# Kernel optimization log

Measured on AMD Instinct MI355X. Metric: run time of the kernel, lower is better.

Reference implementation:

```python
import jax, jax.numpy as jnp
import numpy as np

N = 50000      # nodes
E = 800000     # edges (avg degree 16)
IN = 128       # in_channels
H = 128        # hidden_channels
K = 20         # n_clusters
ALPHA = 0.2


def _glorot(key, shape):
    lim = float(np.sqrt(6.0 / (shape[0] + shape[1])))
    return jax.random.uniform(key, shape, jnp.float32, -lim, lim)


def setup_inputs() -> dict:
    key = jax.random.key(0)
    ks = jax.random.split(key, 12)
    x = jax.random.normal(ks[0], (N, IN), jnp.float32)
    edge_index = jax.random.randint(ks[1], (2, E), 0, N, dtype=jnp.int64)
    edge_weight = jax.random.uniform(ks[2], (E,), jnp.float32)
    perm = jax.random.permutation(ks[3], N).astype(jnp.int64)
    W1 = _glorot(ks[4], (IN, H)); b1 = jnp.zeros((H,), jnp.float32)
    W2 = _glorot(ks[5], (H, H));  b2 = jnp.zeros((H,), jnp.float32)
    W3 = _glorot(ks[6], (H, H));  b3 = jnp.zeros((H,), jnp.float32)
    W4 = _glorot(ks[7], (H, H));  b4 = jnp.zeros((H,), jnp.float32)
    prelu_a = jnp.full((H,), 0.25, jnp.float32)
    Wc = _glorot(ks[8], (H, IN)); bc = jnp.zeros((IN,), jnp.float32)
    mu = jax.random.normal(ks[9], (K, IN), jnp.float32)
    return dict(x=x, edge_index=edge_index, edge_weight=edge_weight, perm=perm,
                W1=W1, b1=b1, W2=W2, b2=b2, W3=W3, b3=b3, W4=W4, b4=b4,
                prelu_a=prelu_a, Wc=Wc, bc=bc, mu=mu)


def _gcn_norm(src, dst, ew, n):
    # add self-loops (weight 1) + symmetric normalization, PyG gcn_norm
    loop = jnp.arange(n)
    src2 = jnp.concatenate([src, loop])
    dst2 = jnp.concatenate([dst, loop])
    w2 = jnp.concatenate([ew, jnp.ones((n,), ew.dtype)])
    deg = jax.ops.segment_sum(w2, dst2, num_segments=n)
    dinv = jnp.where(deg > 0, jax.lax.rsqrt(deg), 0.0)
    norm = dinv[src2] * w2 * dinv[dst2]
    return src2, dst2, norm


def _gcn_conv(x, W, b, src2, dst2, norm, n):
    h = x @ W                              # [n, out]
    msg = h[src2] * norm[:, None]          # gather + scale
    return jax.ops.segment_sum(msg, dst2, num_segments=n) + b


def reference(x, edge_index, edge_weight, perm, W1, b1, W2, b2, W3, b3, W4, b4,
              prelu_a, Wc, bc, mu):
    n = x.shape[0]
    src, dst = edge_index[0], edge_index[1]
    src2, dst2, norm = _gcn_norm(src, dst, edge_weight, n)

    def encoder(h):
        h = _gcn_conv(h, W1, b1, src2, dst2, norm, n)
        h = _gcn_conv(h, W2, b2, src2, dst2, norm, n)
        h = _gcn_conv(h, W3, b3, src2, dst2, norm, n)
        h = _gcn_conv(h, W4, b4, src2, dst2, norm, n)
        return jnp.where(h >= 0, h, prelu_a * h)  # PReLU

    pos_z = encoder(x)
    neg_z = encoder(x[perm])                       # corruption: permute node rows
    summary = jax.nn.sigmoid(pos_z.mean(axis=0))   # [H]

    x_out = _gcn_conv(pos_z, Wc, bc, src2, dst2, norm, n)  # [N, IN]

    # Student's-t soft assignment: ||x_i - mu_k||^2 via expansion (same math)
    d = (jnp.sum(x_out * x_out, axis=1, keepdims=True)
         + jnp.sum(mu * mu, axis=1)[None, :]
         - 2.0 * (x_out @ mu.T))
    d = jnp.maximum(d, 0.0)
    q = 1.0 / (1.0 + d / ALPHA + 1e-8)
    q = q ** (ALPHA + 1.0) / 2.0
    q = q / jnp.sum(q, axis=1, keepdims=True)
    return pos_z, neg_z, summary, x_out, q
```

## Files before the change

kernel.cpp:

```cpp
#include <hip/hip_runtime.h>
#include <hip/hip_bf16.h>

constexpr int NN = 50000;
constexpr int EE = 800000;
constexpr int C  = 128;
constexpr int KC = 20;
constexpr int NB = (NN + 1023) / 1024;

typedef __attribute__((ext_vector_type(8))) short bf16x8;
typedef __attribute__((ext_vector_type(4))) float f32x4;

__device__ inline unsigned short f2bf(float f) {
    unsigned u = __float_as_uint(f);
    u += 0x7fff + ((u >> 16) & 1);
    return (unsigned short)(u >> 16);
}
__device__ inline float bf2f(unsigned short h) {
    return __uint_as_float(((unsigned)h) << 16);
}


__global__ void k_hist(const int* __restrict__ ei, unsigned* cnt) {
    int e = blockIdx.x * 256 + threadIdx.x;
    if (e >= EE) return;
    atomicAdd(&cnt[ei[EE + e]], 1u);
}

__global__ __launch_bounds__(256) void k_scan1(const unsigned* __restrict__ cnt,
                                               unsigned* __restrict__ bsum) {
    __shared__ unsigned red[256];
    int b = blockIdx.x, t = threadIdx.x;
    int i0 = b * 1024 + t * 4;
    unsigned s = 0;
    #pragma unroll
    for (int j = 0; j < 4; ++j) { int i = i0 + j; s += (i < NN) ? cnt[i] : 0u; }
    red[t] = s; __syncthreads();
    for (int st = 128; st > 0; st >>= 1) { if (t < st) red[t] += red[t + st]; __syncthreads(); }
    if (t == 0) bsum[b] = red[0];
}

__global__ void k_scan2(unsigned* bsum, unsigned* total) {
    int t = threadIdx.x;
    unsigned v = (t < NB) ? bsum[t] : 0u;
    unsigned x = v;
    #pragma unroll
    for (int s = 1; s < 64; s <<= 1) { unsigned u = __shfl_up(x, s, 64); if (t >= s) x += u; }
    if (t < NB) bsum[t] = x - v;
    if (t == 63) *total = x;
}

__global__ __launch_bounds__(256) void k_scan3(const unsigned* __restrict__ cnt,
                                               const unsigned* __restrict__ bsum,
                                               const unsigned* __restrict__ total,
                                               unsigned* __restrict__ off,
                                               unsigned* __restrict__ cursor) {
    __shared__ unsigned wred[4];
    int b = blockIdx.x, t = threadIdx.x, lane = t & 63, wv = t >> 6;
    int i0 = b * 1024 + t * 4;
    unsigned v[4]; unsigned s = 0;
    #pragma unroll
    for (int j = 0; j < 4; ++j) { int i = i0 + j; v[j] = (i < NN) ? cnt[i] : 0u; s += v[j]; }
    unsigned x = s;
    #pragma unroll
    for (int st = 1; st < 64; st <<= 1) { unsigned u = __shfl_up(x, st, 64); if (lane >= st) x += u; }
    if (lane == 63) wred[wv] = x;
    __syncthreads();
    unsigned woff = 0;
    for (int k = 0; k < 4; ++k) if (k < wv) woff += wred[k];
    unsigned excl = bsum[b] + woff + x - s;
    #pragma unroll
    for (int j = 0; j < 4; ++j) {
        int i = i0 + j;
        if (i < NN) { off[i] = excl; cursor[i] = excl; excl += v[j]; }
    }
    if (b == 0 && t == 0) off[NN] = *total;
}

__global__ void k_fill(const int* __restrict__ ei, const float* __restrict__ ew,
                       unsigned* cursor, uint2* __restrict__ em) {
    int e = blockIdx.x * 256 + threadIdx.x;
    if (e >= EE) return;
    int s = ei[e];
    int d = ei[EE + e];
    unsigned p = atomicAdd(&cursor[d], 1u);
    em[p] = make_uint2((unsigned)s, __float_as_uint(ew[e]));
}

__global__ void k_dinv_csr(const unsigned* __restrict__ off,
                           const uint2* __restrict__ em, float* __restrict__ dinv) {
    int i = blockIdx.x * 256 + threadIdx.x;
    if (i >= NN) return;
    unsigned p0 = off[i], p1 = off[i + 1];
    float s = 1.0f;
    for (unsigned p = p0; p < p1; ++p) s += __uint_as_float(em[p].y);
    dinv[i] = (s > 0.f) ? rsqrtf(s) : 0.f;
}

__global__ void k_scale(const unsigned* __restrict__ off, const float* __restrict__ dinv,
                        uint2* __restrict__ em) {
    int i = blockIdx.x * 256 + threadIdx.x;
    if (i >= NN) return;
    float di = dinv[i];
    unsigned p0 = off[i], p1 = off[i + 1];
    for (unsigned p = p0; p < p1; ++p) {
        uint2 e = em[p];
        em[p].y = __float_as_uint(dinv[e.x] * __uint_as_float(e.y) * di);
    }
}


__global__ void k_wsplit(const float* W0, const float* W1, const float* W2,
                         const float* W3, const float* W4,
                         unsigned short* __restrict__ wt) {
    int m = blockIdx.x >> 6;
    const float* W = (m == 0) ? W0 : (m == 1) ? W1 : (m == 2) ? W2 : (m == 3) ? W3 : W4;
    int idx = (blockIdx.x & 63) * 256 + threadIdx.x;
    int k = idx >> 7, j = idx & 127;
    float v = W[idx];
    unsigned short h = f2bf(v);
    unsigned short* hi = wt + (size_t)(2 * m) * C * C;
    unsigned short* lo = wt + (size_t)(2 * m + 1) * C * C;
    hi[j * C + k] = h;
    lo[j * C + k] = f2bf(v - bf2f(h));
}

__global__ void k_tobf(const float* __restrict__ x, unsigned short* __restrict__ xb) {
    int i = (blockIdx.x * 256 + threadIdx.x) * 4;
    if (i >= NN * C) return;
    float4 v = *(const float4*)(x + i);
    union { unsigned short u[4]; uint2 p; } o;
    o.u[0] = f2bf(v.x); o.u[1] = f2bf(v.y); o.u[2] = f2bf(v.z); o.u[3] = f2bf(v.w);
    *(uint2*)(xb + i) = o.p;
}


template<bool PERM>
__global__ __launch_bounds__(256) void k_agg(const unsigned short* __restrict__ H,
                                             const int* __restrict__ perm,
                                             const float* __restrict__ dinv,
                                             const unsigned* __restrict__ off,
                                             const uint2* __restrict__ em,
                                             unsigned short* __restrict__ Sh,
                                             unsigned short* __restrict__ Sl) {
    __shared__ uint2 sem[4][64];
    int tid  = threadIdx.x;
    int i    = (blockIdx.x * 256 + tid) >> 6;
    int lane = tid & 63;
    int wid  = tid >> 6;
    if (i >= NN) return;
    int g  = lane >> 4;
    int il = lane & 15;
    const uint4* H4 = (const uint4*)H;

    float a[8];
    {
        int si = PERM ? perm[i] : i;
        uint4 hv = H4[(size_t)si * 16 + il];
        float dv = dinv[i];
        float sn = (g == 0) ? dv * dv : 0.f;
        a[0] = __uint_as_float(hv.x << 16) * sn;
        a[1] = __uint_as_float(hv.x & 0xffff0000u) * sn;
        a[2] = __uint_as_float(hv.y << 16) * sn;
        a[3] = __uint_as_float(hv.y & 0xffff0000u) * sn;
        a[4] = __uint_as_float(hv.z << 16) * sn;
        a[5] = __uint_as_float(hv.z & 0xffff0000u) * sn;
        a[6] = __uint_as_float(hv.w << 16) * sn;
        a[7] = __uint_as_float(hv.w & 0xffff0000u) * sn;
    }

    unsigned p0 = off[i], p1 = off[i + 1];
    for (unsigned base = p0; base < p1; base += 64) {
        unsigned rem = p1 - base;
        int cap = rem < 64u ? (int)rem : 64;
        sem[wid][lane] = em[base + ((unsigned)lane < rem ? (unsigned)lane : 0u)];
        #pragma unroll 4
        for (int t = g; t < cap; t += 4) {
            uint2 e = sem[wid][t];
            unsigned sv = e.x;
            if (PERM) sv = (unsigned)perm[sv];
            float wv = __uint_as_float(e.y);
            uint4 hv = H4[(size_t)sv * 16 + il];
            a[0] += __uint_as_float(hv.x << 16) * wv;
            a[1] += __uint_as_float(hv.x & 0xffff0000u) * wv;
            a[2] += __uint_as_float(hv.y << 16) * wv;
            a[3] += __uint_as_float(hv.y & 0xffff0000u) * wv;
            a[4] += __uint_as_float(hv.z << 16) * wv;
            a[5] += __uint_as_float(hv.z & 0xffff0000u) * wv;
            a[6] += __uint_as_float(hv.w << 16) * wv;
            a[7] += __uint_as_float(hv.w & 0xffff0000u) * wv;
        }
    }

    #pragma unroll
    for (int j = 0; j < 8; ++j) {
        a[j] += __shfl_xor(a[j], 16, 64);
        a[j] += __shfl_xor(a[j], 32, 64);
    }

    if (g < 2) {
        unsigned short h[8], l[8];
        #pragma unroll
        for (int j = 0; j < 8; ++j) {
            h[j] = f2bf(a[j]);
            l[j] = f2bf(a[j] - bf2f(h[j]));
        }
        uint4 o;
        const unsigned short* src = (g == 0) ? h : l;
        o.x = (unsigned)src[0] | ((unsigned)src[1] << 16);
        o.y = (unsigned)src[2] | ((unsigned)src[3] << 16);
        o.z = (unsigned)src[4] | ((unsigned)src[5] << 16);
        o.w = (unsigned)src[6] | ((unsigned)src[7] << 16);
        unsigned short* dst = (g == 0) ? Sh : Sl;
        ((uint4*)dst)[(size_t)i * 16 + il] = o;
    }
}


__global__ __launch_bounds__(256) void k_mm(const unsigned short* __restrict__ Sh,
                                            const unsigned short* __restrict__ Sl,
                                            const unsigned short* __restrict__ Bh,
                                            const unsigned short* __restrict__ Bl,
                                            const float* __restrict__ bias,
                                            const float* __restrict__ prelu,
                                            float* __restrict__ outF,
                                            unsigned short* __restrict__ outB) {
    __shared__ unsigned short Ah[64 * 128];
    __shared__ unsigned short Al[64 * 128];
    int tid  = threadIdx.x;
    int lane = tid & 63;
    int wv   = tid >> 6;
    int row0 = blockIdx.x * 64;

    {
        int r  = tid >> 2;
        int c0 = (tid & 3) * 32;
        int gr = row0 + r;
        bool ok = gr < NN;
        const unsigned short* sH = Sh + (size_t)(ok ? gr : 0) * C + c0;
        const unsigned short* sL = Sl + (size_t)(ok ? gr : 0) * C + c0;
        #pragma unroll
        for (int g = 0; g < 4; ++g) {
            uint4 vh = make_uint4(0, 0, 0, 0), vl = make_uint4(0, 0, 0, 0);
            if (ok) {
                vh = *(const uint4*)(sH + g * 8);
                vl = *(const uint4*)(sL + g * 8);
            }
            int k = c0 + g * 8;
            int byte = (r * 256 + k * 2) ^ ((r & 7) << 4);
            *(uint4*)((char*)Ah + byte) = vh;
            *(uint4*)((char*)Al + byte) = vl;
        }
    }

    bf16x8 bh[2][4], bl[2][4];
    #pragma unroll
    for (int cf = 0; cf < 2; ++cf) {
        int col = wv * 32 + cf * 16 + (lane & 15);
        #pragma unroll
        for (int kt = 0; kt < 4; ++kt) {
            int k = kt * 32 + (lane >> 4) * 8;
            bh[cf][kt] = *(const bf16x8*)(Bh + (size_t)col * C + k);
            bl[cf][kt] = *(const bf16x8*)(Bl + (size_t)col * C + k);
        }
    }

    __syncthreads();

    f32x4 zero = {0.f, 0.f, 0.f, 0.f};
    f32x4 acc[4][2];
    #pragma unroll
    for (int rf = 0; rf < 4; ++rf)
        #pragma unroll
        for (int cf = 0; cf < 2; ++cf) acc[rf][cf] = zero;

    #pragma unroll
    for (int rf = 0; rf < 4; ++rf) {
        int row = rf * 16 + (lane & 15);
        #pragma unroll
        for (int kt = 0; kt < 4; ++kt) {
            int k = kt * 32 + (lane >> 4) * 8;
            int byte = (row * 256 + k * 2) ^ ((row & 7) << 4);
            bf16x8 ah = *(const bf16x8*)((const char*)Ah + byte);
            bf16x8 al = *(const bf16x8*)((const char*)Al + byte);
            #pragma unroll
            for (int cf = 0; cf < 2; ++cf) {
                acc[rf][cf] = __builtin_amdgcn_mfma_f32_16x16x32_bf16(ah, bh[cf][kt], acc[rf][cf], 0, 0, 0);
                acc[rf][cf] = __builtin_amdgcn_mfma_f32_16x16x32_bf16(al, bh[cf][kt], acc[rf][cf], 0, 0, 0);
                acc[rf][cf] = __builtin_amdgcn_mfma_f32_16x16x32_bf16(ah, bl[cf][kt], acc[rf][cf], 0, 0, 0);
            }
        }
    }

    #pragma unroll
    for (int cf = 0; cf < 2; ++cf) {
        int col = wv * 32 + cf * 16 + (lane & 15);
        float bv = bias[col];
        float pv = prelu ? prelu[col] : 0.f;
        #pragma unroll
        for (int rf = 0; rf < 4; ++rf) {
            #pragma unroll
            for (int q = 0; q < 4; ++q) {
                int row = row0 + rf * 16 + (lane >> 4) * 4 + q;
                if (row < NN) {
                    float v = acc[rf][cf][q] + bv;
                    if (prelu) v = (v >= 0.f) ? v : pv * v;
                    if (outF) outF[(size_t)row * C + col] = v;
                    if (outB) outB[(size_t)row * C + col] = f2bf(v);
                }
            }
        }
    }
}


__global__ __launch_bounds__(256) void k_sum(const float* __restrict__ pos, float* sumbuf) {
    __shared__ float red[256];
    int t = threadIdx.x;
    int c = t & 127;
    int half = t >> 7;
    float acc = 0.f;
    for (int r = blockIdx.x * 2 + half; r < NN; r += gridDim.x * 2)
        acc += pos[(size_t)r * C + c];
    red[t] = acc;
    __syncthreads();
    if (half == 0) atomicAdd(&sumbuf[c], acc + red[t + 128]);
}

__global__ void k_summary(const float* sumbuf, float* out) {
    int t = threadIdx.x;
    if (t < C) {
        float m = sumbuf[t] * (1.0f / (float)NN);
        out[t] = 1.0f / (1.0f + expf(-m));
    }
}


__global__ __launch_bounds__(256) void k_q(const float* __restrict__ xo,
                                           const float* __restrict__ mu,
                                           float* __restrict__ qout) {
    __shared__ float sx[64][132];
    __shared__ float smu[KC][128];
    __shared__ float smun[KC];
    int tid = threadIdx.x;
    for (int idx = tid; idx < KC * 128; idx += 256)
        smu[idx >> 7][idx & 127] = mu[idx];
    __syncthreads();
    if (tid < KC) {
        float s = 0.f;
        #pragma unroll 4
        for (int j = 0; j < 128; ++j) { float m = smu[tid][j]; s += m * m; }
        smun[tid] = s;
    }
    int n0 = blockIdx.x * 64;
    for (int idx = tid; idx < 64 * 32; idx += 256) {
        int r = idx >> 5;
        int c = (idx & 31) * 4;
        int gr = n0 + r;
        float4 v = make_float4(0.f, 0.f, 0.f, 0.f);
        if (gr < NN) v = *(const float4*)(xo + (size_t)gr * C + c);
        *(float4*)&sx[r][c] = v;
    }
    __syncthreads();
    int lr = tid >> 2;
    int g  = tid & 3;
    int node = n0 + lr;
    if (node < NN) {
        float ss = 0.f;
        #pragma unroll 8
        for (int j = 0; j < 128; ++j) { float x = sx[lr][j]; ss += x * x; }
        float qv[5]; float qs = 0.f;
        #pragma unroll
        for (int kk = 0; kk < 5; ++kk) {
            int k = g * 5 + kk;
            float dot = 0.f;
            #pragma unroll 8
            for (int j = 0; j < 128; ++j) dot += sx[lr][j] * smu[k][j];
            float d = ss + smun[k] - 2.0f * dot;
            d = fmaxf(d, 0.f);
            float q = 1.0f / (1.0f + d * 5.0f + 1e-8f);
            q = powf(q, 1.2f) * 0.5f;
            qv[kk] = q; qs += q;
        }
        qs += __shfl_xor(qs, 1, 64);
        qs += __shfl_xor(qs, 2, 64);
        float inv = 1.0f / qs;
        #pragma unroll
        for (int kk = 0; kk < 5; ++kk)
            qout[(size_t)node * KC + g * 5 + kk] = qv[kk] * inv;
    }
}


extern "C" void kernel_launch(void* const* d_in, const int* in_sizes, int n_in,
                              void* d_out, int out_size, void* d_ws, size_t ws_size,
                              hipStream_t stream) {
    const float* x    = (const float*)d_in[0];
    const int*   ei   = (const int*)d_in[1];
    const float* ew   = (const float*)d_in[2];
    const int*   perm = (const int*)d_in[3];
    const float* W1 = (const float*)d_in[4];  const float* b1 = (const float*)d_in[5];
    const float* W2 = (const float*)d_in[6];  const float* b2 = (const float*)d_in[7];
    const float* W3 = (const float*)d_in[8];  const float* b3 = (const float*)d_in[9];
    const float* W4 = (const float*)d_in[10]; const float* b4 = (const float*)d_in[11];
    const float* prelu_a = (const float*)d_in[12];
    const float* Wc = (const float*)d_in[13]; const float* bc = (const float*)d_in[14];
    const float* mu = (const float*)d_in[15];

    float* out     = (float*)d_out;
    float* pos_z   = out;
    float* neg_z   = out + (size_t)NN * C;
    float* summary = out + (size_t)2 * NN * C;
    float* xout    = summary + C;
    float* qout    = xout + (size_t)NN * C;

    char* w = (char*)d_ws;
    auto carve = [&](size_t bytes) { void* p = (void*)w; w += (bytes + 511) & ~(size_t)511; return p; };
    float*          dinv   = (float*)carve((size_t)NN * 4);
    unsigned*       cnt    = (unsigned*)carve((size_t)(NN + 1) * 4);
    unsigned*       cursor = (unsigned*)carve((size_t)NN * 4);
    unsigned*       bsum   = (unsigned*)carve(256 * 4);
    unsigned*       total  = (unsigned*)carve(64);
    uint2*          em     = (uint2*)carve((size_t)EE * 8);
    float*          sumbuf = (float*)carve(512);
    unsigned short* wt     = (unsigned short*)carve((size_t)5 * 2 * C * C * 2);
    unsigned short* B0     = (unsigned short*)carve((size_t)NN * C * 2);
    unsigned short* B1     = (unsigned short*)carve((size_t)NN * C * 2);
    unsigned short* B2     = (unsigned short*)carve((size_t)NN * C * 2);
    unsigned short* ShP    = (unsigned short*)carve((size_t)NN * C * 2);
    unsigned short* SlP    = (unsigned short*)carve((size_t)NN * C * 2);

    unsigned short* Wh[5], *Wl[5];
    for (int m = 0; m < 5; ++m) {
        Wh[m] = wt + (size_t)(2 * m) * C * C;
        Wl[m] = wt + (size_t)(2 * m + 1) * C * C;
    }

    hipMemsetAsync(cnt, 0, (size_t)(NN + 1) * 4, stream);
    hipMemsetAsync(sumbuf, 0, 512, stream);

    int gE = (EE + 255) / 256, gN = (NN + 255) / 256;

    k_hist <<<gE, 256, 0, stream>>>(ei, cnt);
    k_scan1<<<NB, 256, 0, stream>>>(cnt, bsum);
    k_scan2<<<1, 64, 0, stream>>>(bsum, total);
    k_scan3<<<NB, 256, 0, stream>>>(cnt, bsum, total, cnt, cursor);
    k_fill <<<gE, 256, 0, stream>>>(ei, ew, cursor, em);
    k_dinv_csr<<<gN, 256, 0, stream>>>(cnt, em, dinv);
    k_scale<<<gN, 256, 0, stream>>>(cnt, dinv, em);

    k_wsplit<<<320, 256, 0, stream>>>(W1, W2, W3, W4, Wc, wt);
    k_tobf  <<<(NN * C / 4 + 255) / 256, 256, 0, stream>>>(x, B0);

    int gA = (NN + 3) / 4;
    int gM = (NN + 63) / 64;

    auto layer = [&](const unsigned short* src, const int* prm, int wm,
                     const float* b, const float* pr, float* oF, unsigned short* oB) {
        if (prm)
            k_agg<true><<<gA, 256, 0, stream>>>(src, prm, dinv, cnt, em, ShP, SlP);
        else
            k_agg<false><<<gA, 256, 0, stream>>>(src, nullptr, dinv, cnt, em, ShP, SlP);
        k_mm<<<gM, 256, 0, stream>>>(ShP, SlP, Wh[wm], Wl[wm], b, pr, oF, oB);
    };

    layer(B0, perm,    0, b1, nullptr, nullptr, B2);
    layer(B0, nullptr, 0, b1, nullptr, nullptr, B1);
    layer(B1, nullptr, 1, b2, nullptr, nullptr, B0);
    layer(B0, nullptr, 2, b3, nullptr, nullptr, B1);
    layer(B1, nullptr, 3, b4, prelu_a, pos_z,   B0);
    layer(B2, nullptr, 1, b2, nullptr, nullptr, B1);
    layer(B1, nullptr, 2, b3, nullptr, nullptr, B2);
    layer(B2, nullptr, 3, b4, prelu_a, neg_z,   nullptr);
    layer(B0, nullptr, 4, bc, nullptr, xout,    nullptr);

    k_sum<<<256, 256, 0, stream>>>(pos_z, sumbuf);
    k_summary<<<1, 128, 0, stream>>>(sumbuf, summary);

    k_q<<<(NN + 63) / 64, 256, 0, stream>>>(xout, mu, qout);
}
```

Baseline: 675.8 us.

## Reorder GCN layers to transform-then-aggregate and batch pos/neg chains per launch

```diff
diff --git a/kernel.cpp b/kernel.cpp
--- a/kernel.cpp
+++ b/kernel.cpp
@@ -124,37 +124,212 @@
     lo[j * C + k] = f2bf(v - bf2f(h));
 }
 
-__global__ void k_tobf(const float* __restrict__ x, unsigned short* __restrict__ xb) {
-    int i = (blockIdx.x * 256 + threadIdx.x) * 4;
-    if (i >= NN * C) return;
-    float4 v = *(const float4*)(x + i);
-    union { unsigned short u[4]; uint2 p; } o;
-    o.u[0] = f2bf(v.x); o.u[1] = f2bf(v.y); o.u[2] = f2bf(v.z); o.u[3] = f2bf(v.w);
-    *(uint2*)(xb + i) = o.p;
-}
-
-
-template<bool PERM>
-__global__ __launch_bounds__(256) void k_agg(const unsigned short* __restrict__ H,
-                                             const int* __restrict__ perm,
-                                             const float* __restrict__ dinv,
-                                             const unsigned* __restrict__ off,
-                                             const uint2* __restrict__ em,
-                                             unsigned short* __restrict__ Sh,
-                                             unsigned short* __restrict__ Sl) {
+
+__global__ __launch_bounds__(256) void k_mm_f32(const float* __restrict__ A,
+                                                const unsigned short* __restrict__ Bh,
+                                                const unsigned short* __restrict__ Bl,
+                                                unsigned short* __restrict__ G) {
+    __shared__ unsigned short Ah[64 * 128];
+    __shared__ unsigned short Al[64 * 128];
+    int tid  = threadIdx.x;
+    int lane = tid & 63;
+    int wv   = tid >> 6;
+    int row0 = blockIdx.x * 64;
+
+    {
+        int r  = tid >> 2;
+        int c0 = (tid & 3) * 32;
+        int gr = row0 + r;
+        bool ok = gr < NN;
+        const float* src = A + (size_t)(ok ? gr : 0) * C + c0;
+        #pragma unroll
+        for (int g = 0; g < 4; ++g) {
+            float f[8];
+            if (ok) {
+                *(float4*)&f[0] = *(const float4*)(src + g * 8);
+                *(float4*)&f[4] = *(const float4*)(src + g * 8 + 4);
+            } else {
+                #pragma unroll
+                for (int j = 0; j < 8; ++j) f[j] = 0.f;
+            }
+            union { unsigned short u[8]; uint4 v; } ph, pl;
+            #pragma unroll
+            for (int j = 0; j < 8; ++j) {
+                unsigned short h = f2bf(f[j]);
+                ph.u[j] = h;
+                pl.u[j] = f2bf(f[j] - bf2f(h));
+            }
+            int k = c0 + g * 8;
+            int byte = (r * 256 + k * 2) ^ ((r & 7) << 4);
+            *(uint4*)((char*)Ah + byte) = ph.v;
+            *(uint4*)((char*)Al + byte) = pl.v;
+        }
+    }
+
+    bf16x8 bh[2][4], bl[2][4];
+    #pragma unroll
+    for (int cf = 0; cf < 2; ++cf) {
+        int col = wv * 32 + cf * 16 + (lane & 15);
+        #pragma unroll
+        for (int kt = 0; kt < 4; ++kt) {
+            int k = kt * 32 + (lane >> 4) * 8;
+            bh[cf][kt] = *(const bf16x8*)(Bh + (size_t)col * C + k);
+            bl[cf][kt] = *(const bf16x8*)(Bl + (size_t)col * C + k);
+        }
+    }
+
+    __syncthreads();
+
+    f32x4 zero = {0.f, 0.f, 0.f, 0.f};
+    f32x4 acc[4][2];
+    #pragma unroll
+    for (int rf = 0; rf < 4; ++rf)
+        #pragma unroll
+        for (int cf = 0; cf < 2; ++cf) acc[rf][cf] = zero;
+
+    #pragma unroll
+    for (int rf = 0; rf < 4; ++rf) {
+        int row = rf * 16 + (lane & 15);
+        #pragma unroll
+        for (int kt = 0; kt < 4; ++kt) {
+            int k = kt * 32 + (lane >> 4) * 8;
+            int byte = (row * 256 + k * 2) ^ ((row & 7) << 4);
+            bf16x8 ah = *(const bf16x8*)((const char*)Ah + byte);
+            bf16x8 al = *(const bf16x8*)((const char*)Al + byte);
+            #pragma unroll
+            for (int cf = 0; cf < 2; ++cf) {
+                acc[rf][cf] = __builtin_amdgcn_mfma_f32_16x16x32_bf16(ah, bh[cf][kt], acc[rf][cf], 0, 0, 0);
+                acc[rf][cf] = __builtin_amdgcn_mfma_f32_16x16x32_bf16(al, bh[cf][kt], acc[rf][cf], 0, 0, 0);
+                acc[rf][cf] = __builtin_amdgcn_mfma_f32_16x16x32_bf16(ah, bl[cf][kt], acc[rf][cf], 0, 0, 0);
+            }
+        }
+    }
+
+    #pragma unroll
+    for (int cf = 0; cf < 2; ++cf) {
+        int col = wv * 32 + cf * 16 + (lane & 15);
+        #pragma unroll
+        for (int rf = 0; rf < 4; ++rf) {
+            #pragma unroll
+            for (int q = 0; q < 4; ++q) {
+                int row = row0 + rf * 16 + (lane >> 4) * 4 + q;
+                if (row < NN) G[(size_t)row * C + col] = f2bf(acc[rf][cf][q]);
+            }
+        }
+    }
+}
+
+
+__global__ __launch_bounds__(256) void k_mm2(const unsigned short* __restrict__ Ap,
+                                             const unsigned short* __restrict__ An,
+                                             const unsigned short* __restrict__ Bh,
+                                             const unsigned short* __restrict__ Bl,
+                                             unsigned short* __restrict__ Gp,
+                                             unsigned short* __restrict__ Gn, int nblk) {
+    __shared__ unsigned short Ah[64 * 128];
+    int tid  = threadIdx.x;
+    int lane = tid & 63;
+    int wv   = tid >> 6;
+    int chain = blockIdx.x >= nblk;
+    int blk   = chain ? blockIdx.x - nblk : blockIdx.x;
+    const unsigned short* A = chain ? An : Ap;
+    unsigned short*       G = chain ? Gn : Gp;
+    int row0 = blk * 64;
+
+    {
+        int r  = tid >> 2;
+        int c0 = (tid & 3) * 32;
+        int gr = row0 + r;
+        bool ok = gr < NN;
+        const unsigned short* s = A + (size_t)(ok ? gr : 0) * C + c0;
+        #pragma unroll
+        for (int g = 0; g < 4; ++g) {
+            uint4 v = ok ? *(const uint4*)(s + g * 8) : make_uint4(0, 0, 0, 0);
+            int k = c0 + g * 8;
+            int byte = (r * 256 + k * 2) ^ ((r & 7) << 4);
+            *(uint4*)((char*)Ah + byte) = v;
+        }
+    }
+
+    bf16x8 bh[2][4], bl[2][4];
+    #pragma unroll
+    for (int cf = 0; cf < 2; ++cf) {
+        int col = wv * 32 + cf * 16 + (lane & 15);
+        #pragma unroll
+        for (int kt = 0; kt < 4; ++kt) {
+            int k = kt * 32 + (lane >> 4) * 8;
+            bh[cf][kt] = *(const bf16x8*)(Bh + (size_t)col * C + k);
+            bl[cf][kt] = *(const bf16x8*)(Bl + (size_t)col * C + k);
+        }
+    }
+
+    __syncthreads();
+
+    f32x4 zero = {0.f, 0.f, 0.f, 0.f};
+    f32x4 acc[4][2];
+    #pragma unroll
+    for (int rf = 0; rf < 4; ++rf)
+        #pragma unroll
+        for (int cf = 0; cf < 2; ++cf) acc[rf][cf] = zero;
+
+    #pragma unroll
+    for (int rf = 0; rf < 4; ++rf) {
+        int row = rf * 16 + (lane & 15);
+        #pragma unroll
+        for (int kt = 0; kt < 4; ++kt) {
+            int k = kt * 32 + (lane >> 4) * 8;
+            int byte = (row * 256 + k * 2) ^ ((row & 7) << 4);
+            bf16x8 a = *(const bf16x8*)((const char*)Ah + byte);
+            #pragma unroll
+            for (int cf = 0; cf < 2; ++cf) {
+                acc[rf][cf] = __builtin_amdgcn_mfma_f32_16x16x32_bf16(a, bh[cf][kt], acc[rf][cf], 0, 0, 0);
+                acc[rf][cf] = __builtin_amdgcn_mfma_f32_16x16x32_bf16(a, bl[cf][kt], acc[rf][cf], 0, 0, 0);
+            }
+        }
+    }
+
+    #pragma unroll
+    for (int cf = 0; cf < 2; ++cf) {
+        int col = wv * 32 + cf * 16 + (lane & 15);
+        #pragma unroll
+        for (int rf = 0; rf < 4; ++rf) {
+            #pragma unroll
+            for (int q = 0; q < 4; ++q) {
+                int row = row0 + rf * 16 + (lane >> 4) * 4 + q;
+                if (row < NN) G[(size_t)row * C + col] = f2bf(acc[rf][cf][q]);
+            }
+        }
+    }
+}
+
+
+__global__ __launch_bounds__(256) void k_agg2(const unsigned short* __restrict__ Gp,
+                                              const unsigned short* __restrict__ Gn,
+                                              const int* __restrict__ permN,
+                                              const float* __restrict__ dinv,
+                                              const unsigned* __restrict__ off,
+                                              const uint2* __restrict__ em,
+                                              const float* __restrict__ bias,
+                                              const float* __restrict__ prelu,
+                                              unsigned short* planeP, unsigned short* planeN,
+                                              float* fP, float* fN, int nb) {
     __shared__ uint2 sem[4][64];
-    int tid  = threadIdx.x;
-    int i    = (blockIdx.x * 256 + tid) >> 6;
-    int lane = tid & 63;
-    int wid  = tid >> 6;
+    int tid   = threadIdx.x;
+    int chain = blockIdx.x >= nb;
+    int blk   = chain ? blockIdx.x - nb : blockIdx.x;
+    int i     = (blk * 256 + tid) >> 6;
+    int lane  = tid & 63;
+    int wid   = tid >> 6;
     if (i >= NN) return;
+    const unsigned short* Gsel = chain ? Gn : Gp;
+    const int*            prm  = chain ? permN : nullptr;
     int g  = lane >> 4;
     int il = lane & 15;
-    const uint4* H4 = (const uint4*)H;
+    const uint4* H4 = (const uint4*)Gsel;
 
     float a[8];
     {
-        int si = PERM ? perm[i] : i;
+        int si = prm ? prm[i] : i;
         uint4 hv = H4[(size_t)si * 16 + il];
         float dv = dinv[i];
         float sn = (g == 0) ? dv * dv : 0.f;
@@ -177,7 +352,7 @@
         for (int t = g; t < cap; t += 4) {
             uint2 e = sem[wid][t];
             unsigned sv = e.x;
-            if (PERM) sv = (unsigned)perm[sv];
+            if (prm) sv = (unsigned)prm[sv];
             float wv = __uint_as_float(e.y);
             uint4 hv = H4[(size_t)sv * 16 + il];
             a[0] += __uint_as_float(hv.x << 16) * wv;
@@ -197,118 +372,34 @@
         a[j] += __shfl_xor(a[j], 32, 64);
     }
 
-    if (g < 2) {
-        unsigned short h[8], l[8];
-        #pragma unroll
-        for (int j = 0; j < 8; ++j) {
-            h[j] = f2bf(a[j]);
-            l[j] = f2bf(a[j] - bf2f(h[j]));
-        }
+    {
+        float bv[8];
+        *(float4*)&bv[0] = *(const float4*)(bias + il * 8);
+        *(float4*)&bv[4] = *(const float4*)(bias + il * 8 + 4);
+        #pragma unroll
+        for (int j = 0; j < 8; ++j) a[j] += bv[j];
+        if (prelu) {
+            float pv[8];
+            *(float4*)&pv[0] = *(const float4*)(prelu + il * 8);
+            *(float4*)&pv[4] = *(const float4*)(prelu + il * 8 + 4);
+            #pragma unroll
+            for (int j = 0; j < 8; ++j) a[j] = (a[j] >= 0.f) ? a[j] : pv[j] * a[j];
+        }
+    }
+
+    unsigned short* plane = chain ? planeN : planeP;
+    float*          fo    = chain ? fN : fP;
+    if (g == 0 && plane) {
         uint4 o;
-        const unsigned short* src = (g == 0) ? h : l;
-        o.x = (unsigned)src[0] | ((unsigned)src[1] << 16);
-        o.y = (unsigned)src[2] | ((unsigned)src[3] << 16);
-        o.z = (unsigned)src[4] | ((unsigned)src[5] << 16);
-        o.w = (unsigned)src[6] | ((unsigned)src[7] << 16);
-        unsigned short* dst = (g == 0) ? Sh : Sl;
-        ((uint4*)dst)[(size_t)i * 16 + il] = o;
-    }
-}
-
-
-__global__ __launch_bounds__(256) void k_mm(const unsigned short* __restrict__ Sh,
-                                            const unsigned short* __restrict__ Sl,
-                                            const unsigned short* __restrict__ Bh,
-                                            const unsigned short* __restrict__ Bl,
-                                            const float* __restrict__ bias,
-                                            const float* __restrict__ prelu,
-                                            float* __restrict__ outF,
-                                            unsigned short* __restrict__ outB) {
-    __shared__ unsigned short Ah[64 * 128];
-    __shared__ unsigned short Al[64 * 128];
-    int tid  = threadIdx.x;
-    int lane = tid & 63;
-    int wv   = tid >> 6;
-    int row0 = blockIdx.x * 64;
-
-    {
-        int r  = tid >> 2;
-        int c0 = (tid & 3) * 32;
-        int gr = row0 + r;
-        bool ok = gr < NN;
-        const unsigned short* sH = Sh + (size_t)(ok ? gr : 0) * C + c0;
-        const unsigned short* sL = Sl + (size_t)(ok ? gr : 0) * C + c0;
-        #pragma unroll
-        for (int g = 0; g < 4; ++g) {
-            uint4 vh = make_uint4(0, 0, 0, 0), vl = make_uint4(0, 0, 0, 0);
-            if (ok) {
-                vh = *(const uint4*)(sH + g * 8);
-                vl = *(const uint4*)(sL + g * 8);
-            }
-            int k = c0 + g * 8;
-            int byte = (r * 256 + k * 2) ^ ((r & 7) << 4);
-            *(uint4*)((char*)Ah + byte) = vh;
-            *(uint4*)((char*)Al + byte) = vl;
-        }
-    }
-
-    bf16x8 bh[2][4], bl[2][4];
-    #pragma unroll
-    for (int cf = 0; cf < 2; ++cf) {
-        int col = wv * 32 + cf * 16 + (lane & 15);
-        #pragma unroll
-        for (int kt = 0; kt < 4; ++kt) {
-            int k = kt * 32 + (lane >> 4) * 8;
-            bh[cf][kt] = *(const bf16x8*)(Bh + (size_t)col * C + k);
-            bl[cf][kt] = *(const bf16x8*)(Bl + (size_t)col * C + k);
-        }
-    }
-
-    __syncthreads();
-
-    f32x4 zero = {0.f, 0.f, 0.f, 0.f};
-    f32x4 acc[4][2];
-    #pragma unroll
-    for (int rf = 0; rf < 4; ++rf)
-        #pragma unroll
-        for (int cf = 0; cf < 2; ++cf) acc[rf][cf] = zero;
-
-    #pragma unroll
-    for (int rf = 0; rf < 4; ++rf) {
-        int row = rf * 16 + (lane & 15);
-        #pragma unroll
-        for (int kt = 0; kt < 4; ++kt) {
-            int k = kt * 32 + (lane >> 4) * 8;
-            int byte = (row * 256 + k * 2) ^ ((row & 7) << 4);
-            bf16x8 ah = *(const bf16x8*)((const char*)Ah + byte);
-            bf16x8 al = *(const bf16x8*)((const char*)Al + byte);
-            #pragma unroll
-            for (int cf = 0; cf < 2; ++cf) {
-                acc[rf][cf] = __builtin_amdgcn_mfma_f32_16x16x32_bf16(ah, bh[cf][kt], acc[rf][cf], 0, 0, 0);
-                acc[rf][cf] = __builtin_amdgcn_mfma_f32_16x16x32_bf16(al, bh[cf][kt], acc[rf][cf], 0, 0, 0);
-                acc[rf][cf] = __builtin_amdgcn_mfma_f32_16x16x32_bf16(ah, bl[cf][kt], acc[rf][cf], 0, 0, 0);
-            }
-        }
-    }
-
-    #pragma unroll
-    for (int cf = 0; cf < 2; ++cf) {
-        int col = wv * 32 + cf * 16 + (lane & 15);
-        float bv = bias[col];
-        float pv = prelu ? prelu[col] : 0.f;
-        #pragma unroll
-        for (int rf = 0; rf < 4; ++rf) {
-            #pragma unroll
-            for (int q = 0; q < 4; ++q) {
-                int row = row0 + rf * 16 + (lane >> 4) * 4 + q;
-                if (row < NN) {
-                    float v = acc[rf][cf][q] + bv;
-                    if (prelu) v = (v >= 0.f) ? v : pv * v;
-                    if (outF) outF[(size_t)row * C + col] = v;
-                    if (outB) outB[(size_t)row * C + col] = f2bf(v);
-                }
-            }
-        }
+        o.x = (unsigned)f2bf(a[0]) | ((unsigned)f2bf(a[1]) << 16);
+        o.y = (unsigned)f2bf(a[2]) | ((unsigned)f2bf(a[3]) << 16);
+        o.z = (unsigned)f2bf(a[4]) | ((unsigned)f2bf(a[5]) << 16);
+        o.w = (unsigned)f2bf(a[6]) | ((unsigned)f2bf(a[7]) << 16);
+        ((uint4*)plane)[(size_t)i * 16 + il] = o;
+    }
+    if (fo) {
+        if (g == 1) *(float4*)(fo + (size_t)i * C + il * 8)     = make_float4(a[0], a[1], a[2], a[3]);
+        if (g == 2) *(float4*)(fo + (size_t)i * C + il * 8 + 4) = make_float4(a[4], a[5], a[6], a[7]);
     }
 }
 
@@ -423,11 +514,11 @@
     uint2*          em     = (uint2*)carve((size_t)EE * 8);
     float*          sumbuf = (float*)carve(512);
     unsigned short* wt     = (unsigned short*)carve((size_t)5 * 2 * C * C * 2);
-    unsigned short* B0     = (unsigned short*)carve((size_t)NN * C * 2);
-    unsigned short* B1     = (unsigned short*)carve((size_t)NN * C * 2);
-    unsigned short* B2     = (unsigned short*)carve((size_t)NN * C * 2);
-    unsigned short* ShP    = (unsigned short*)carve((size_t)NN * C * 2);
-    unsigned short* SlP    = (unsigned short*)carve((size_t)NN * C * 2);
+    unsigned short* Gp     = (unsigned short*)carve((size_t)NN * C * 2);
+    unsigned short* Gn     = (unsigned short*)carve((size_t)NN * C * 2);
+    unsigned short* P0     = (unsigned short*)carve((size_t)NN * C * 2);
+    unsigned short* P1     = (unsigned short*)carve((size_t)NN * C * 2);
+    unsigned short* P2     = (unsigned short*)carve((size_t)NN * C * 2);
 
     unsigned short* Wh[5], *Wl[5];
     for (int m = 0; m < 5; ++m) {
@@ -449,29 +540,25 @@
     k_scale<<<gN, 256, 0, stream>>>(cnt, dinv, em);
 
     k_wsplit<<<320, 256, 0, stream>>>(W1, W2, W3, W4, Wc, wt);
-    k_tobf  <<<(NN * C / 4 + 255) / 256, 256, 0, stream>>>(x, B0);
-
+
+    int gM = (NN + 63) / 64;
     int gA = (NN + 3) / 4;
-    int gM = (NN + 63) / 64;
-
-    auto layer = [&](const unsigned short* src, const int* prm, int wm,
-                     const float* b, const float* pr, float* oF, unsigned short* oB) {
-        if (prm)
-            k_agg<true><<<gA, 256, 0, stream>>>(src, prm, dinv, cnt, em, ShP, SlP);
-        else
-            k_agg<false><<<gA, 256, 0, stream>>>(src, nullptr, dinv, cnt, em, ShP, SlP);
-        k_mm<<<gM, 256, 0, stream>>>(ShP, SlP, Wh[wm], Wl[wm], b, pr, oF, oB);
-    };
-
-    layer(B0, perm,    0, b1, nullptr, nullptr, B2);
-    layer(B0, nullptr, 0, b1, nullptr, nullptr, B1);
-    layer(B1, nullptr, 1, b2, nullptr, nullptr, B0);
-    layer(B0, nullptr, 2, b3, nullptr, nullptr, B1);
-    layer(B1, nullptr, 3, b4, prelu_a, pos_z,   B0);
-    layer(B2, nullptr, 1, b2, nullptr, nullptr, B1);
-    layer(B1, nullptr, 2, b3, nullptr, nullptr, B2);
-    layer(B2, nullptr, 3, b4, prelu_a, neg_z,   nullptr);
-    layer(B0, nullptr, 4, bc, nullptr, xout,    nullptr);
+
+    k_mm_f32<<<gM, 256, 0, stream>>>(x, Wh[0], Wl[0], Gp);
+    k_agg2<<<2 * gA, 256, 0, stream>>>(Gp, Gp, perm, dinv, cnt, em, b1, nullptr,
+                                       P0, P1, nullptr, nullptr, gA);
+    k_mm2 <<<2 * gM, 256, 0, stream>>>(P0, P1, Wh[1], Wl[1], Gp, Gn, gM);
+    k_agg2<<<2 * gA, 256, 0, stream>>>(Gp, Gn, nullptr, dinv, cnt, em, b2, nullptr,
+                                       P0, P1, nullptr, nullptr, gA);
+    k_mm2 <<<2 * gM, 256, 0, stream>>>(P0, P1, Wh[2], Wl[2], Gp, Gn, gM);
+    k_agg2<<<2 * gA, 256, 0, stream>>>(Gp, Gn, nullptr, dinv, cnt, em, b3, nullptr,
+                                       P0, P1, nullptr, nullptr, gA);
+    k_mm2 <<<2 * gM, 256, 0, stream>>>(P0, P1, Wh[3], Wl[3], Gp, Gn, gM);
+    k_agg2<<<2 * gA, 256, 0, stream>>>(Gp, Gn, nullptr, dinv, cnt, em, b4, prelu_a,
+                                       P2, nullptr, pos_z, neg_z, gA);
+    k_mm2 <<<gM, 256, 0, stream>>>(P2, P2, Wh[4], Wl[4], Gp, Gn, gM);
+    k_agg2<<<gA, 256, 0, stream>>>(Gp, Gp, nullptr, dinv, cnt, em, bc, nullptr,
+                                   nullptr, nullptr, xout, nullptr, gA);
 
     k_sum<<<256, 256, 0, stream>>>(pos_z, sumbuf);
     k_summary<<<1, 128, 0, stream>>>(sumbuf, summary);
```

Result: faster. 600.4 us (-11.2%).
